# Kernel optimization log

Measured on AMD Instinct MI355X. Metric: run time of the kernel, lower is better.

## Reference

```python
import jax, jax.numpy as jnp
import numpy as np


def setup_inputs() -> dict:
    key = jax.random.key(0)
    ks = jax.random.split(key, 4)
    B, C, H, W = 8, 256, 64, 64
    C8 = C // 8
    x = jax.random.normal(ks[0], (B, C, H, W), dtype=jnp.float32)
    wq = jax.random.normal(ks[1], (C8, C), dtype=jnp.float32) * 0.05
    wk = jax.random.normal(ks[2], (C8, C), dtype=jnp.float32) * 0.05
    wv = jax.random.normal(ks[3], (C, C), dtype=jnp.float32) * 0.05
    bq = jnp.zeros((C8,), jnp.float32)
    bk = jnp.zeros((C8,), jnp.float32)
    bv = jnp.zeros((C,), jnp.float32)
    return {"x": x, "wq": wq, "bq": bq, "wk": wk, "bk": bk, "wv": wv, "bv": bv}


def _conv1x1(x, w, b):
    # x: [B,C,H,W], w: [O,C], b: [O] -> [B,O,H,W]
    return jnp.einsum('bchw,oc->bohw', x, w) + b[None, :, None, None]


def reference(x, wq, bq, wk, bk, wv, bv):
    B, C, H, W = x.shape
    N = H * W
    q = _conv1x1(x, wq, bq).reshape(B, -1, N)   # [B, C/8, N]
    k = _conv1x1(x, wk, bk).reshape(B, -1, N)   # [B, C/8, N]
    v = _conv1x1(x, wv, bv).reshape(B, C, N)    # [B, C, N]
    # energy[b, n, m] = sum_c q[b, c, n] * k[b, c, m]
    energy = jnp.einsum('bcn,bcm->bnm', q, k)   # [B, N, N]
    attn = jax.nn.softmax(energy, axis=-1)
    # out[b, c, n] = sum_m v[b, c, m] * attn[b, n, m]
    out = jnp.einsum('bcm,bnm->bcn', v, attn)   # [B, C, N]
    return out.reshape(B, C, H, W) + x
```

## Files before the change

### kernel.cpp

```cpp
#include <hip/hip_runtime.h>

#define B_ 8
#define C_ 256
#define C8_ 32
#define N_ 4096

typedef __bf16 bf16;
typedef __bf16 bf16x4 __attribute__((ext_vector_type(4)));
typedef __bf16 bf16x8 __attribute__((ext_vector_type(8)));
typedef float f32x4 __attribute__((ext_vector_type(4)));
typedef float f32x16 __attribute__((ext_vector_type(16)));

#if __has_builtin(__builtin_amdgcn_exp2f)
#define EXP2 __builtin_amdgcn_exp2f
#else
#define EXP2 exp2f
#endif

#define CVTPK(lo, hi) ({ unsigned int _w;                                     \
  asm("v_cvt_pk_bf16_f32 %0, %1, %2" : "=v"(_w) : "v"(lo), "v"(hi)); _w; })
#define LSWAP(a, b) asm("v_permlane32_swap_b32 %0, %1" : "+v"(a), "+v"(b))

#define GLD16(gp, lp) __builtin_amdgcn_global_load_lds(                       \
    (const __attribute__((address_space(1))) void*)(gp),                      \
    (__attribute__((address_space(3))) void*)(lp), 16, 0, 0)
#define VMW(n) do { asm volatile("s_waitcnt vmcnt(" n ")" ::: "memory");      \
    __builtin_amdgcn_sched_barrier(0); } while (0)
#define RBAR() __builtin_amdgcn_s_barrier()

__global__ __launch_bounds__(256) void k_transpose(const float* __restrict__ x,
    bf16* __restrict__ xT, const float* __restrict__ wq,
    const float* __restrict__ wk, const float* __restrict__ wv,
    bf16* __restrict__ Wb) {
  __shared__ bf16 t[64][72];
  int bid = blockIdx.x;
  int tid = threadIdx.x;
  if (bid < 80) {
    int i = (bid * 256 + tid) * 4;
    const float* src; int off;
    if (i < 8192) { src = wq; off = i; }
    else if (i < 16384) { src = wk; off = i - 8192; }
    else { src = wv; off = i - 16384; }
    f32x4 v = *reinterpret_cast<const f32x4*>(src + off);
    bf16x4 o;
    o[0] = (bf16)v[0]; o[1] = (bf16)v[1]; o[2] = (bf16)v[2]; o[3] = (bf16)v[3];
    *reinterpret_cast<bf16x4*>(Wb + i) = o;
  }
  int b = bid & 7, rem = bid >> 3;
  int c0 = (rem >> 6) * 64, n0 = (rem & 63) * 64;
#pragma unroll
  for (int r = 0; r < 4; ++r) {
    int cc = r * 16 + (tid >> 4);
    int j = (tid & 15) * 4;
    f32x4 v = *reinterpret_cast<const f32x4*>(
        x + ((size_t)b * C_ + c0 + cc) * N_ + n0 + j);
    bf16x4 o;
    o[0] = (bf16)v[0]; o[1] = (bf16)v[1]; o[2] = (bf16)v[2]; o[3] = (bf16)v[3];
    *reinterpret_cast<bf16x4*>(&t[cc][j]) = o;
  }
  __syncthreads();
#pragma unroll
  for (int r = 0; r < 2; ++r) {
    int nn = r * 32 + (tid >> 3);
    int c8 = (tid & 7) * 8;
    bf16x8 o;
#pragma unroll
    for (int k = 0; k < 8; ++k) o[k] = t[c8 + k][nn];
    *reinterpret_cast<bf16x8*>(
        xT + ((size_t)b * N_ + n0 + nn) * C_ + c0 + c8) = o;
  }
}

__global__ __launch_bounds__(256) void k_proj(const bf16* __restrict__ xT,
    const bf16* __restrict__ Wb, const float* __restrict__ bq,
    const float* __restrict__ bk, const float* __restrict__ bv,
    bf16* __restrict__ Qt, bf16* __restrict__ Kt, bf16* __restrict__ Vt) {
  int bid = blockIdx.x;
  int b = bid & 7, nt = bid >> 3;
  int tid = threadIdx.x, lane = tid & 63, w = tid >> 6;
  int ln = lane & 31, h = lane >> 5;
  int nsub = w & 1, og = w >> 1;
  int n0 = nt * 64 + nsub * 32;
  const bf16* xp = xT + ((size_t)b * N_ + n0 + ln) * C_ + h * 8;

  bf16x8 xf[16];
#pragma unroll
  for (int k = 0; k < 16; ++k) xf[k] = *reinterpret_cast<const bf16x8*>(xp + k * 16);

  if (og == 0) {
    {
      const bf16* wp = Wb + (size_t)ln * C_ + h * 8;
      bf16x8 wf[16];
#pragma unroll
      for (int k = 0; k < 16; ++k) wf[k] = *reinterpret_cast<const bf16x8*>(wp + k * 16);
      f32x16 acc;
#pragma unroll
      for (int r = 0; r < 16; ++r) acc[r] = 0.f;
#pragma unroll
      for (int k = 0; k < 16; ++k)
        acc = __builtin_amdgcn_mfma_f32_32x32x16_bf16(xf[k], wf[k], acc, 0, 0, 0);
      float bb = bq[ln];
#pragma unroll
      for (int r = 0; r < 16; ++r) {
        int n = n0 + (r & 3) + 8 * (r >> 2) + 4 * h;
        Qt[((size_t)b * N_ + n) * C8_ + ln] = (bf16)((acc[r] + bb) * 1.44269504f);
      }
    }
    {
      const bf16* wp = Wb + 8192 + (size_t)ln * C_ + h * 8;
      bf16x8 wf[16];
#pragma unroll
      for (int k = 0; k < 16; ++k) wf[k] = *reinterpret_cast<const bf16x8*>(wp + k * 16);
      f32x16 acc;
#pragma unroll
      for (int r = 0; r < 16; ++r) acc[r] = 0.f;
#pragma unroll
      for (int k = 0; k < 16; ++k)
        acc = __builtin_amdgcn_mfma_f32_32x32x16_bf16(xf[k], wf[k], acc, 0, 0, 0);
      float bb = bk[ln];
      int f = (ln >> 4) & 1, hA = (ln >> 3) & 1, e = ln & 7;
#pragma unroll
      for (int r = 0; r < 16; ++r) {
        int n = n0 + (r & 3) + 8 * (r >> 2) + 4 * h;
        int mt = n >> 5, lm = n & 31;
        Kt[((size_t)(b * 128 + mt) * 2 + f) * 512 + (lm + hA * 32) * 8 + e] =
            (bf16)(acc[r] + bb);
      }
    }
  }
  int mt = n0 >> 5;
  bf16* tb = Vt + (size_t)(b * 128 + mt) * 8192;
  int j2 = (ln >> 4) & 1, hA = (ln >> 3) & 1, e = ln & 7;
  int ot0 = og ? 3 : 0;
  int ot1 = og ? 8 : 3;
#pragma unroll 1
  for (int ot = ot0; ot < ot1; ++ot) {
    const bf16* wp = Wb + 16384 + (size_t)(ot * 32 + ln) * C_ + h * 8;
    bf16x8 wf[16];
#pragma unroll
    for (int k = 0; k < 16; ++k) wf[k] = *reinterpret_cast<const bf16x8*>(wp + k * 16);
    f32x16 acc;
#pragma unroll
    for (int r = 0; r < 16; ++r) acc[r] = 0.f;
#pragma unroll
    for (int k = 0; k < 16; ++k)
      acc = __builtin_amdgcn_mfma_f32_32x32x16_bf16(wf[k], xf[k], acc, 0, 0, 0);
#pragma unroll
    for (int r = 0; r < 16; ++r) {
      int cc = (r & 3) + 8 * (r >> 2) + 4 * h;
      tb[(ot * 2 + j2) * 512 + (cc + hA * 32) * 8 + e] =
          (bf16)(acc[r] + bv[ot * 32 + cc]);
    }
  }
}

__global__ __launch_bounds__(256, 2) void k_attn(const bf16* __restrict__ Qt,
    const bf16* __restrict__ Kt, const bf16* __restrict__ Vt,
    const float* __restrict__ x, float* __restrict__ out) {
  __shared__ __align__(16) char sbuf[67584];
  __shared__ float sML[2][2][32];
  int bid = blockIdx.x;
  int b = bid & 7;
  int qt = bid >> 3;
  int tid = threadIdx.x, lane = tid & 63, w = tid >> 6;
  int ln = lane & 31, h = lane >> 5;
  int qh = w & 1, mh = w >> 1;
  int n0 = qt * 64 + qh * 32;
  char* bufs = sbuf + mh * 32768;

  const bf16* qp = Qt + ((size_t)b * N_ + n0 + ln) * C8_ + h * 8;
  bf16x8 qf0 = *reinterpret_cast<const bf16x8*>(qp);
  bf16x8 qf1 = *reinterpret_cast<const bf16x8*>(qp + 16);
  const bf16* Kb = Kt + (size_t)(b * 128 + mh * 64) * 1024 + (size_t)lane * 8;
  const char* Vg = (const char*)(Vt + (size_t)(b * 128 + mh * 64) * 8192)
                   + (size_t)lane * 16;

  f32x16 o[8];
#pragma unroll
  for (int ct = 0; ct < 8; ++ct)
#pragma unroll
    for (int r = 0; r < 16; ++r) o[ct][r] = 0.f;
  float L = 0.f;

  bf16x8 kf0 = *reinterpret_cast<const bf16x8*>(Kb);
  bf16x8 kf1 = *reinterpret_cast<const bf16x8*>(Kb + 512);
#pragma unroll
  for (int f = 0; f < 8; ++f)
    GLD16(Vg + (qh * 8 + f) * 1024, bufs + (qh * 8 + f) * 1024);
  VMW("8");

  int pp = 0;
#pragma unroll 1
  for (int it = 0; it < 64; ++it) {
    int itn = it + 1 > 63 ? 63 : it + 1;
    bf16x8 kn0 = *reinterpret_cast<const bf16x8*>(Kb + (size_t)itn * 1024);
    bf16x8 kn1 = *reinterpret_cast<const bf16x8*>(Kb + (size_t)itn * 1024 + 512);

    f32x16 s;
#pragma unroll
    for (int r = 0; r < 16; ++r) s[r] = 0.f;
    s = __builtin_amdgcn_mfma_f32_32x32x16_bf16(kf0, qf0, s, 0, 0, 0);
    s = __builtin_amdgcn_mfma_f32_32x32x16_bf16(kf1, qf1, s, 0, 0, 0);

#pragma unroll
    for (int r = 0; r < 16; ++r) s[r] = EXP2(s[r]);
    float q0 = (s[0] + s[1]) + (s[2] + s[3]);
    float q1 = (s[4] + s[5]) + (s[6] + s[7]);
    float q2 = (s[8] + s[9]) + (s[10] + s[11]);
    float q3 = (s[12] + s[13]) + (s[14] + s[15]);
    L += (q0 + q1) + (q2 + q3);

    unsigned int c0 = CVTPK(s[0], s[1]),   c1 = CVTPK(s[2], s[3]);
    unsigned int c2 = CVTPK(s[4], s[5]),   c3 = CVTPK(s[6], s[7]);
    unsigned int c4 = CVTPK(s[8], s[9]),   c5 = CVTPK(s[10], s[11]);
    unsigned int c6 = CVTPK(s[12], s[13]), c7 = CVTPK(s[14], s[15]);
    LSWAP(c0, c2); LSWAP(c1, c3); LSWAP(c4, c6); LSWAP(c5, c7);
    union { unsigned int u[4]; bf16x8 v; } P0, P1;
    P0.u[0] = c0; P0.u[1] = c1; P0.u[2] = c2; P0.u[3] = c3;
    P1.u[0] = c4; P1.u[1] = c5; P1.u[2] = c6; P1.u[3] = c7;

    VMW("2");
    RBAR();

    char* bc = bufs + pp * 16384;
    __builtin_amdgcn_s_setprio(1);
#pragma unroll
    for (int ct = 0; ct < 8; ++ct) {
      bf16x8 vf0 = *reinterpret_cast<const bf16x8*>(bc + (2 * ct) * 1024 + lane * 16);
      bf16x8 vf1 = *reinterpret_cast<const bf16x8*>(bc + (2 * ct + 1) * 1024 + lane * 16);
      o[ct] = __builtin_amdgcn_mfma_f32_32x32x16_bf16(vf0, P0.v, o[ct], 0, 0, 0);
      o[ct] = __builtin_amdgcn_mfma_f32_32x32x16_bf16(vf1, P1.v, o[ct], 0, 0, 0);
    }
    __builtin_amdgcn_s_setprio(0);

    const char* vg = Vg + (size_t)itn * 16384;
    char* bn = bufs + (pp ^ 1) * 16384;
#pragma unroll
    for (int f = 0; f < 8; ++f)
      GLD16(vg + (qh * 8 + f) * 1024, bn + (qh * 8 + f) * 1024);

    kf0 = kn0; kf1 = kn1;
    pp ^= 1;
  }
  VMW("0");

  L += __shfl_xor(L, 32);
  if (lane < 32) sML[mh][qh][lane] = L;
  __syncthreads();
  float (*Ob)[256][33] = reinterpret_cast<float (*)[256][33]>(sbuf);
  float inv = 1.f / (sML[0][qh][ln] + sML[1][qh][ln]);
  if (mh) {
#pragma unroll
    for (int ct = 0; ct < 8; ++ct)
#pragma unroll
      for (int r = 0; r < 16; ++r) {
        int c = ct * 32 + (r & 3) + 8 * (r >> 2) + 4 * h;
        Ob[qh][c][ln] = o[ct][r];
      }
  }
  __syncthreads();
  if (!mh) {
#pragma unroll
    for (int ct = 0; ct < 8; ++ct)
#pragma unroll
      for (int r = 0; r < 16; ++r) {
        int c = ct * 32 + (r & 3) + 8 * (r >> 2) + 4 * h;
        size_t idx = ((size_t)b * C_ + c) * N_ + n0 + ln;
        out[idx] = (o[ct][r] + Ob[qh][c][ln]) * inv + x[idx];
      }
  }
}

extern "C" void kernel_launch(void* const* d_in, const int* in_sizes, int n_in,
                              void* d_out, int out_size, void* d_ws, size_t ws_size,
                              hipStream_t stream) {
  const float* x  = (const float*)d_in[0];
  const float* wq = (const float*)d_in[1];
  const float* bq = (const float*)d_in[2];
  const float* wk = (const float*)d_in[3];
  const float* bk = (const float*)d_in[4];
  const float* wv = (const float*)d_in[5];
  const float* bv = (const float*)d_in[6];
  float* out = (float*)d_out;

  bf16* xT = (bf16*)d_ws;
  bf16* Qt = xT + (size_t)B_ * N_ * C_;
  bf16* Kt = Qt + (size_t)B_ * N_ * C8_;
  bf16* Vt = Kt + (size_t)B_ * N_ * C8_;
  bf16* Wb = Vt + (size_t)B_ * N_ * C_;

  k_transpose<<<dim3(2048), dim3(256), 0, stream>>>(x, xT, wq, wk, wv, Wb);
  k_proj<<<dim3(512), dim3(256), 0, stream>>>(xT, Wb, bq, bk, bv, Qt, Kt, Vt);
  k_attn<<<dim3(512), dim3(256), 0, stream>>>(Qt, Kt, Vt, x, out);
}
```

Before: 134.9 us.

## Switch attention to 16x16x32 MFMA tiles with smaller query blocks and single V buffer

```diff
diff --git a/kernel.cpp b/kernel.cpp
--- a/kernel.cpp
+++ b/kernel.cpp
@@ -20,6 +20,7 @@
 #define CVTPK(lo, hi) ({ unsigned int _w;                                     \
   asm("v_cvt_pk_bf16_f32 %0, %1, %2" : "=v"(_w) : "v"(lo), "v"(hi)); _w; })
 #define LSWAP(a, b) asm("v_permlane32_swap_b32 %0, %1" : "+v"(a), "+v"(b))
+#define LSWAP16(a, b) asm("v_permlane16_swap_b32 %0, %1" : "+v"(a), "+v"(b))
 
 #define GLD16(gp, lp) __builtin_amdgcn_global_load_lds(                       \
     (const __attribute__((address_space(1))) void*)(gp),                      \
@@ -87,6 +88,7 @@
 #pragma unroll
   for (int k = 0; k < 16; ++k) xf[k] = *reinterpret_cast<const bf16x8*>(xp + k * 16);
 
+  int mt = n0 >> 5;
   if (og == 0) {
     {
       const bf16* wp = Wb + (size_t)ln * C_ + h * 8;
@@ -118,19 +120,19 @@
       for (int k = 0; k < 16; ++k)
         acc = __builtin_amdgcn_mfma_f32_32x32x16_bf16(xf[k], wf[k], acc, 0, 0, 0);
       float bb = bk[ln];
-      int f = (ln >> 4) & 1, hA = (ln >> 3) & 1, e = ln & 7;
+      bf16* kb = Kt + (size_t)(b * 128 + mt) * 1024;
+      int e = ln & 7, gc = ln >> 3;
 #pragma unroll
       for (int r = 0; r < 16; ++r) {
-        int n = n0 + (r & 3) + 8 * (r >> 2) + 4 * h;
-        int mt = n >> 5, lm = n & 31;
-        Kt[((size_t)(b * 128 + mt) * 2 + f) * 512 + (lm + hA * 32) * 8 + e] =
-            (bf16)(acc[r] + bb);
-      }
-    }
-  }
-  int mt = n0 >> 5;
+        int m_local = (r & 3) + 8 * (r >> 2) + 4 * h;
+        int f = m_local >> 4;
+        int Ld = (m_local & 15) | (gc << 4);
+        kb[f * 512 + Ld * 8 + e] = (bf16)(acc[r] + bb);
+      }
+    }
+  }
   bf16* tb = Vt + (size_t)(b * 128 + mt) * 8192;
-  int j2 = (ln >> 4) & 1, hA = (ln >> 3) & 1, e = ln & 7;
+  int e = ln & 7, gm = ln >> 3;
   int ot0 = og ? 3 : 0;
   int ot1 = og ? 8 : 3;
 #pragma unroll 1
@@ -148,125 +150,115 @@
 #pragma unroll
     for (int r = 0; r < 16; ++r) {
       int cc = (r & 3) + 8 * (r >> 2) + 4 * h;
-      tb[(ot * 2 + j2) * 512 + (cc + hA * 32) * 8 + e] =
-          (bf16)(acc[r] + bv[ot * 32 + cc]);
-    }
-  }
-}
-
-__global__ __launch_bounds__(256, 2) void k_attn(const bf16* __restrict__ Qt,
+      int c = ot * 32 + cc;
+      int ct = c >> 4;
+      int Ld = (c & 15) | (gm << 4);
+      tb[ct * 512 + Ld * 8 + e] = (bf16)(acc[r] + bv[c]);
+    }
+  }
+}
+
+__global__ __launch_bounds__(256, 3) void k_attn(const bf16* __restrict__ Qt,
     const bf16* __restrict__ Kt, const bf16* __restrict__ Vt,
     const float* __restrict__ x, float* __restrict__ out) {
-  __shared__ __align__(16) char sbuf[67584];
-  __shared__ float sML[2][2][32];
+  __shared__ __align__(16) char sbuf[34816];
+  __shared__ float sML[2][2][16];
   int bid = blockIdx.x;
   int b = bid & 7;
-  int qt = bid >> 3;
+  int qb = bid >> 3;
   int tid = threadIdx.x, lane = tid & 63, w = tid >> 6;
-  int ln = lane & 31, h = lane >> 5;
+  int qq = lane & 15, g = lane >> 4;
   int qh = w & 1, mh = w >> 1;
-  int n0 = qt * 64 + qh * 32;
-  char* bufs = sbuf + mh * 32768;
-
-  const bf16* qp = Qt + ((size_t)b * N_ + n0 + ln) * C8_ + h * 8;
-  bf16x8 qf0 = *reinterpret_cast<const bf16x8*>(qp);
-  bf16x8 qf1 = *reinterpret_cast<const bf16x8*>(qp + 16);
+  int n0 = qb * 32 + qh * 16;
+  char* Vbuf = sbuf + mh * 16384;
+
+  bf16x8 qf = *reinterpret_cast<const bf16x8*>(
+      Qt + ((size_t)b * N_ + n0 + qq) * C8_ + g * 8);
   const bf16* Kb = Kt + (size_t)(b * 128 + mh * 64) * 1024 + (size_t)lane * 8;
   const char* Vg = (const char*)(Vt + (size_t)(b * 128 + mh * 64) * 8192)
-                   + (size_t)lane * 16;
-
-  f32x16 o[8];
-#pragma unroll
-  for (int ct = 0; ct < 8; ++ct)
-#pragma unroll
-    for (int r = 0; r < 16; ++r) o[ct][r] = 0.f;
+                   + qh * 8192 + (size_t)lane * 16;
+  char* Vdst = Vbuf + qh * 8192;
+
+  f32x4 o[16];
+#pragma unroll
+  for (int ct = 0; ct < 16; ++ct)
+#pragma unroll
+    for (int j = 0; j < 4; ++j) o[ct][j] = 0.f;
   float L = 0.f;
 
   bf16x8 kf0 = *reinterpret_cast<const bf16x8*>(Kb);
   bf16x8 kf1 = *reinterpret_cast<const bf16x8*>(Kb + 512);
 #pragma unroll
-  for (int f = 0; f < 8; ++f)
-    GLD16(Vg + (qh * 8 + f) * 1024, bufs + (qh * 8 + f) * 1024);
-  VMW("8");
-
-  int pp = 0;
+  for (int f = 0; f < 8; ++f) GLD16(Vg + f * 1024, Vdst + f * 1024);
+
 #pragma unroll 1
   for (int it = 0; it < 64; ++it) {
     int itn = it + 1 > 63 ? 63 : it + 1;
     bf16x8 kn0 = *reinterpret_cast<const bf16x8*>(Kb + (size_t)itn * 1024);
     bf16x8 kn1 = *reinterpret_cast<const bf16x8*>(Kb + (size_t)itn * 1024 + 512);
 
-    f32x16 s;
-#pragma unroll
-    for (int r = 0; r < 16; ++r) s[r] = 0.f;
-    s = __builtin_amdgcn_mfma_f32_32x32x16_bf16(kf0, qf0, s, 0, 0, 0);
-    s = __builtin_amdgcn_mfma_f32_32x32x16_bf16(kf1, qf1, s, 0, 0, 0);
-
-#pragma unroll
-    for (int r = 0; r < 16; ++r) s[r] = EXP2(s[r]);
-    float q0 = (s[0] + s[1]) + (s[2] + s[3]);
-    float q1 = (s[4] + s[5]) + (s[6] + s[7]);
-    float q2 = (s[8] + s[9]) + (s[10] + s[11]);
-    float q3 = (s[12] + s[13]) + (s[14] + s[15]);
-    L += (q0 + q1) + (q2 + q3);
-
-    unsigned int c0 = CVTPK(s[0], s[1]),   c1 = CVTPK(s[2], s[3]);
-    unsigned int c2 = CVTPK(s[4], s[5]),   c3 = CVTPK(s[6], s[7]);
-    unsigned int c4 = CVTPK(s[8], s[9]),   c5 = CVTPK(s[10], s[11]);
-    unsigned int c6 = CVTPK(s[12], s[13]), c7 = CVTPK(s[14], s[15]);
-    LSWAP(c0, c2); LSWAP(c1, c3); LSWAP(c4, c6); LSWAP(c5, c7);
-    union { unsigned int u[4]; bf16x8 v; } P0, P1;
-    P0.u[0] = c0; P0.u[1] = c1; P0.u[2] = c2; P0.u[3] = c3;
-    P1.u[0] = c4; P1.u[1] = c5; P1.u[2] = c6; P1.u[3] = c7;
+    f32x4 s0, s1;
+#pragma unroll
+    for (int j = 0; j < 4; ++j) { s0[j] = 0.f; s1[j] = 0.f; }
+    s0 = __builtin_amdgcn_mfma_f32_16x16x32_bf16(kf0, qf, s0, 0, 0, 0);
+    s1 = __builtin_amdgcn_mfma_f32_16x16x32_bf16(kf1, qf, s1, 0, 0, 0);
+
+#pragma unroll
+    for (int j = 0; j < 4; ++j) { s0[j] = EXP2(s0[j]); s1[j] = EXP2(s1[j]); }
+    L += ((s0[0] + s0[1]) + (s0[2] + s0[3]))
+       + ((s1[0] + s1[1]) + (s1[2] + s1[3]));
+
+    unsigned int w0 = CVTPK(s0[0], s0[1]), w1 = CVTPK(s0[2], s0[3]);
+    unsigned int w2 = CVTPK(s1[0], s1[1]), w3 = CVTPK(s1[2], s1[3]);
+    LSWAP(w0, w2); LSWAP(w1, w3);
+    LSWAP16(w0, w2); LSWAP16(w1, w3);
+    union { unsigned int u[4]; bf16x8 v; } P;
+    P.u[0] = w0; P.u[1] = w1; P.u[2] = w2; P.u[3] = w3;
 
     VMW("2");
     RBAR();
 
-    char* bc = bufs + pp * 16384;
     __builtin_amdgcn_s_setprio(1);
 #pragma unroll
-    for (int ct = 0; ct < 8; ++ct) {
-      bf16x8 vf0 = *reinterpret_cast<const bf16x8*>(bc + (2 * ct) * 1024 + lane * 16);
-      bf16x8 vf1 = *reinterpret_cast<const bf16x8*>(bc + (2 * ct + 1) * 1024 + lane * 16);
-      o[ct] = __builtin_amdgcn_mfma_f32_32x32x16_bf16(vf0, P0.v, o[ct], 0, 0, 0);
-      o[ct] = __builtin_amdgcn_mfma_f32_32x32x16_bf16(vf1, P1.v, o[ct], 0, 0, 0);
+    for (int ct = 0; ct < 16; ++ct) {
+      bf16x8 vf = *reinterpret_cast<const bf16x8*>(Vbuf + ct * 1024 + lane * 16);
+      o[ct] = __builtin_amdgcn_mfma_f32_16x16x32_bf16(vf, P.v, o[ct], 0, 0, 0);
     }
     __builtin_amdgcn_s_setprio(0);
+    RBAR();
 
     const char* vg = Vg + (size_t)itn * 16384;
-    char* bn = bufs + (pp ^ 1) * 16384;
-#pragma unroll
-    for (int f = 0; f < 8; ++f)
-      GLD16(vg + (qh * 8 + f) * 1024, bn + (qh * 8 + f) * 1024);
+#pragma unroll
+    for (int f = 0; f < 8; ++f) GLD16(vg + f * 1024, Vdst + f * 1024);
 
     kf0 = kn0; kf1 = kn1;
-    pp ^= 1;
   }
   VMW("0");
 
+  L += __shfl_xor(L, 16);
   L += __shfl_xor(L, 32);
-  if (lane < 32) sML[mh][qh][lane] = L;
+  if (lane < 16) sML[mh][qh][lane] = L;
   __syncthreads();
-  float (*Ob)[256][33] = reinterpret_cast<float (*)[256][33]>(sbuf);
-  float inv = 1.f / (sML[0][qh][ln] + sML[1][qh][ln]);
+  float (*Ob)[256][17] = reinterpret_cast<float (*)[256][17]>(sbuf);
+  float inv = 1.f / (sML[0][qh][qq] + sML[1][qh][qq]);
   if (mh) {
 #pragma unroll
-    for (int ct = 0; ct < 8; ++ct)
-#pragma unroll
-      for (int r = 0; r < 16; ++r) {
-        int c = ct * 32 + (r & 3) + 8 * (r >> 2) + 4 * h;
-        Ob[qh][c][ln] = o[ct][r];
+    for (int ct = 0; ct < 16; ++ct)
+#pragma unroll
+      for (int j = 0; j < 4; ++j) {
+        int c = ct * 16 + g * 4 + j;
+        Ob[qh][c][qq] = o[ct][j];
       }
   }
   __syncthreads();
   if (!mh) {
 #pragma unroll
-    for (int ct = 0; ct < 8; ++ct)
-#pragma unroll
-      for (int r = 0; r < 16; ++r) {
-        int c = ct * 32 + (r & 3) + 8 * (r >> 2) + 4 * h;
-        size_t idx = ((size_t)b * C_ + c) * N_ + n0 + ln;
-        out[idx] = (o[ct][r] + Ob[qh][c][ln]) * inv + x[idx];
+    for (int ct = 0; ct < 16; ++ct)
+#pragma unroll
+      for (int j = 0; j < 4; ++j) {
+        int c = ct * 16 + g * 4 + j;
+        size_t idx = ((size_t)b * C_ + c) * N_ + n0 + qq;
+        out[idx] = (o[ct][j] + Ob[qh][c][qq]) * inv + x[idx];
       }
   }
 }
@@ -291,5 +283,5 @@
 
   k_transpose<<<dim3(2048), dim3(256), 0, stream>>>(x, xT, wq, wk, wv, Wb);
   k_proj<<<dim3(512), dim3(256), 0, stream>>>(xT, Wb, bq, bk, bv, Qt, Kt, Vt);
-  k_attn<<<dim3(512), dim3(256), 0, stream>>>(Qt, Kt, Vt, x, out);
-}
+  k_attn<<<dim3(1024), dim3(256), 0, stream>>>(Qt, Kt, Vt, x, out);
+}
```

After: 156.2 us. +15.7%, slower.
